# Kernel optimization log

Hardware: AMD Instinct MI355X
Metric: run time of the kernel (lower is better)

## Reference

```python
import jax, jax.numpy as jnp
import numpy as np

T, B, S, D = 512, 32, 512, 512
EPS = 1e-6  # LayerNorm eps


def _ln(x, g, b):
    m = jnp.mean(x, axis=-1, keepdims=True)
    v = jnp.mean((x - m) ** 2, axis=-1, keepdims=True)
    return g * (x - m) * jax.lax.rsqrt(v + EPS) + b


def setup_inputs() -> dict:
    key = jax.random.key(0)
    ks = jax.random.split(key, 10)
    sc = 1.0 / np.sqrt(D).astype(np.float32)
    return {
        "prev_layer": jax.random.normal(ks[0], (T, B, D), jnp.float32),
        "hidden": jax.random.normal(ks[1], (B, D), jnp.float32),
        "enc_output": jax.random.normal(ks[2], (B, S, D), jnp.float32),
        "memory_length": jax.random.randint(ks[3], (B,), 1, S + 1),
        # nn.Linear weights stored as [in, out] (transposed torch layout)
        "W_in": jax.random.normal(ks[4], (D, 3 * D), jnp.float32) * sc,
        "W_enc": jax.random.normal(ks[5], (D, D), jnp.float32) * sc,
        "W_attn_in": jax.random.normal(ks[6], (D, D), jnp.float32) * sc,
        "W_hidden": jax.random.normal(ks[7], (D, D), jnp.float32) * sc,
        "W_ctx": jax.random.normal(ks[8], (D, D), jnp.float32) * sc,
        # LayerNorm gains/biases (5 LNs)
        "g_pre": jnp.ones((3 * D,), jnp.float32), "b_pre": jnp.zeros((3 * D,), jnp.float32),
        "g_enc": jnp.ones((D,), jnp.float32), "b_enc": jnp.zeros((D,), jnp.float32),
        "g_attn": jnp.ones((D,), jnp.float32), "b_attn": jnp.zeros((D,), jnp.float32),
        "g_h": jnp.ones((D,), jnp.float32), "b_h": jnp.zeros((D,), jnp.float32),
        "g_c": jnp.ones((D,), jnp.float32), "b_c": jnp.zeros((D,), jnp.float32),
    }


def reference(prev_layer, hidden, enc_output, W_in, W_enc, W_attn_in, W_hidden,
              W_ctx, g_pre, b_pre, g_enc, b_enc, g_attn, b_attn, g_h, b_h,
              g_c, b_c, memory_length):
    d = prev_layer.shape[-1]
    sqrt_d = jnp.sqrt(jnp.asarray(d, prev_layer.dtype))
    # dropout is identity in eval mode
    preact = _ln(prev_layer @ W_in, g_pre, b_pre)          # [T,B,3D]
    pctx = _ln(enc_output @ W_enc, g_enc, b_enc)           # [B,S,D]
    z, h_gate, pl_t = jnp.split(preact, 3, axis=-1)
    z = jax.nn.sigmoid(z)
    h_gate = jax.nn.sigmoid(h_gate)

    # SRU-style linear recurrence: s_t = (1-z_t)*s_{t-1} + z_t*pl_t
    def step(h, zp):
        z_t, p_t = zp
        s = (1.0 - z_t) * h + z_t * p_t
        return s, s

    hidden_last, ss = jax.lax.scan(step, hidden, (z, pl_t))  # ss: [T,B,D]

    attn_in = _ln(ss @ W_attn_in, g_attn, b_attn)            # [T,B,D]
    align = jnp.einsum('tbd,bsd->bts', attn_in, pctx)        # [B,T,S]
    mask = jnp.arange(pctx.shape[1])[None, :] < memory_length[:, None]  # [B,S]
    align = jnp.where(mask[:, None, :], align, -jnp.inf)
    av = jax.nn.softmax(align / sqrt_d, axis=-1)             # [B,T,S]
    c = jnp.einsum('bts,bsd->tbd', av, pctx)                 # [T,B,D]
    attn_out = c / sqrt_d

    trans = _ln(ss @ W_hidden, g_h, b_h) + _ln(attn_out @ W_ctx, g_c, b_c)
    out = jnp.tanh(trans)
    out = (1.0 - h_gate) * out + h_gate * prev_layer         # [T,B,D]
    p_attn = jnp.transpose(av, (1, 0, 2))                    # [T,B,S]
    return out, hidden_last, p_attn
```

## Files before the change

### kernel.cpp

```cpp
#include <hip/hip_runtime.h>
#include <hip/hip_bf16.h>
#include <cmath>

#define T_ 512
#define B_ 32
#define S_ 512
#define D_ 512
#define D3_ 1536
#define NCH 16
#define CT (T_ / NCH)
static constexpr float LN_EPS = 1e-6f;
static constexpr float RSQRT_D = 0.044194173824159216f;

typedef __attribute__((ext_vector_type(8))) __bf16 bf16x8;
typedef __attribute__((ext_vector_type(4))) float f32x4;

struct __align__(8) bfx4 { __hip_bfloat16 x, y, z, w; };

__device__ __forceinline__ void g2l16(const void* g, void* l) {
    __builtin_amdgcn_global_load_lds(
        (const __attribute__((address_space(1))) unsigned int*)g,
        (__attribute__((address_space(3))) unsigned int*)l, 16, 0, 0);
}

__device__ __forceinline__ float xr_sum16(float v) {
    v += __shfl_xor(v, 1); v += __shfl_xor(v, 2);
    v += __shfl_xor(v, 4); v += __shfl_xor(v, 8); return v;
}
__device__ __forceinline__ float xr_max16(float v) {
    v = fmaxf(v, __shfl_xor(v, 1)); v = fmaxf(v, __shfl_xor(v, 2));
    v = fmaxf(v, __shfl_xor(v, 4)); v = fmaxf(v, __shfl_xor(v, 8)); return v;
}

__device__ __forceinline__ float sigmoidf_(float x) {
    return 1.f / (1.f + __expf(-x));
}
__device__ __forceinline__ float sigmoid_fast(float x) {
    return __fdividef(1.f, 1.f + __expf(-x));
}
__device__ __forceinline__ float tanh_fast(float x) {
    return 1.f - __fdividef(2.f, __expf(2.f * x) + 1.f);
}
__device__ __forceinline__ float bfu(unsigned short u) {
    unsigned int v = ((unsigned int)u) << 16;
    return __uint_as_float(v);
}

__global__ __launch_bounds__(256) void gemm_pre(
    const __hip_bfloat16* __restrict__ A,
    const __hip_bfloat16* __restrict__ Bw,
    __hip_bfloat16* __restrict__ preb,
    float2* __restrict__ part)
{
    __shared__ char smem[32768];

    const int lin = blockIdx.y * 12 + blockIdx.x;
    const int swz = (lin & 7) * 192 + (lin >> 3);
    const int bx = swz % 12, by = swz / 12;
    const int m0 = by * 128, n0 = bx * 128;
    const int tid = threadIdx.x, lane = tid & 63, w = tid >> 6;
    const int wm = (w >> 1) * 64, wn = (w & 1) * 64;
    const int srow = lane >> 2, skB = (lane & 3) * 16;
    const int q = lane >> 4, c = lane & 15;

    f32x4 acc[4][4];
#pragma unroll
    for (int i = 0; i < 4; i++)
#pragma unroll
        for (int j = 0; j < 4; j++) acc[i][j] = (f32x4)(0.0f);

    const char* ga0 = (const char*)(A + (long)(m0 + w * 16 + srow) * 512) + skB;
    const char* ga1 = (const char*)(A + (long)(m0 + (w + 4) * 16 + srow) * 512) + skB;
    const char* gb0 = (const char*)(Bw + (long)(n0 + w * 16 + srow) * 512) + skB;
    const char* gb1 = (const char*)(Bw + (long)(n0 + (w + 4) * 16 + srow) * 512) + skB;
    char* la0 = smem + w * 1024 + lane * 16;
    char* la1 = smem + (w + 4) * 1024 + lane * 16;
    char* lb0 = smem + 8192 + w * 1024 + lane * 16;
    char* lb1 = smem + 8192 + (w + 4) * 1024 + lane * 16;
    const char* Ar = smem + (wm + c) * 64 + q * 16;
    const char* Br = smem + 8192 + (wn + c) * 64 + q * 16;

    g2l16(ga0, la0);
    g2l16(ga1, la1);
    g2l16(gb0, lb0);
    g2l16(gb1, lb1);
    __syncthreads();

#pragma unroll
    for (int kk = 0; kk < 16; kk++) {
        const int cb = (kk & 1) << 14;
        const int nb = cb ^ 16384;
        if (kk < 15) {
            const long kb = (long)(kk + 1) * 64;
            g2l16(ga0 + kb, la0 + nb);
            g2l16(ga1 + kb, la1 + nb);
            g2l16(gb0 + kb, lb0 + nb);
            g2l16(gb1 + kb, lb1 + nb);
        }
        bf16x8 af[4], bfr[4];
#pragma unroll
        for (int i = 0; i < 4; i++) {
            af[i] = *(const bf16x8*)(Ar + cb + i * 1024);
            bfr[i] = *(const bf16x8*)(Br + cb + i * 1024);
        }
#pragma unroll
        for (int i = 0; i < 4; i++)
#pragma unroll
            for (int j = 0; j < 4; j++)
                acc[i][j] = __builtin_amdgcn_mfma_f32_16x16x32_bf16(
                    af[i], bfr[j], acc[i][j], 0, 0, 0);
        __syncthreads();
    }

    float2* sred = (float2*)smem;
#pragma unroll
    for (int i = 0; i < 4; i++)
#pragma unroll
        for (int r = 0; r < 4; r++) {
            float s = 0.f, qq = 0.f;
#pragma unroll
            for (int j = 0; j < 4; j++) {
                float v = acc[i][j][r]; s += v; qq += v * v;
            }
            s = xr_sum16(s); qq = xr_sum16(qq);
            if (c == 0) sred[(wm + i * 16 + q * 4 + r) * 2 + (w & 1)] =
                make_float2(s, qq);
        }
    __syncthreads();
    if ((w & 1) == 0 && c == 0) {
#pragma unroll
        for (int i = 0; i < 4; i++)
#pragma unroll
            for (int r = 0; r < 4; r++) {
                int row = wm + i * 16 + q * 4 + r;
                float2 a = sred[row * 2], b2 = sred[row * 2 + 1];
                part[(long)bx * 16384 + m0 + row] =
                    make_float2(a.x + b2.x, a.y + b2.y);
            }
    }
    __syncthreads();

    for (int p = 0; p < 2; p++) {
        if ((w >> 1) == p) {
#pragma unroll
            for (int i = 0; i < 4; i++)
#pragma unroll
                for (int j = 0; j < 4; j++)
#pragma unroll
                    for (int r = 0; r < 4; r++) {
                        int row = i * 16 + q * 4 + r;
                        int col = wn + j * 16 + c;
                        ((__hip_bfloat16*)smem)[row * 128 + col] =
                            __float2bfloat16(acc[i][j][r]);
                    }
        }
        __syncthreads();
#pragma unroll
        for (int rnd = 0; rnd < 4; rnd++) {
            int row = rnd * 16 + (tid >> 4);
            int ch = tid & 15;
            uint4 v = *(const uint4*)(smem + row * 256 + ch * 16);
            long grow = m0 + p * 64 + row;
            *(uint4*)((char*)preb + grow * 3072 + (long)n0 * 2 + ch * 16) = v;
        }
        __syncthreads();
    }
}

#define RC_BUF 34816
__device__ __forceinline__ void rows_core32(
    const __hip_bfloat16* A, long lda,
    const __hip_bfloat16* B, long ldb,
    char* smem, f32x4 (&acc)[2][8])
{
    const int tid = threadIdx.x, lane = tid & 63, w = tid >> 6;
#pragma unroll
    for (int m = 0; m < 2; m++)
#pragma unroll
        for (int j = 0; j < 8; j++) acc[m][j] = (f32x4)(0.0f);

    const char* ga = (const char*)(A + (long)(w * 16 + (lane >> 2)) * lda) + (lane & 3) * 16;
    char* la = smem + w * 1024 + lane * 16;
    const char* gb = (const char*)(B + (long)(w * 128 + (lane >> 2)) * ldb) + (lane & 3) * 16;
    char* lb = smem + 2048 + w * 8192 + lane * 16;
    const long ldbB16 = (long)ldb * 32;
    const char* Ar = smem + (lane & 15) * 64 + (lane >> 4) * 16;
    const char* Br = smem + 2048 + (w * 128 + (lane & 15)) * 64 + (lane >> 4) * 16;

    if (w < 2) g2l16(ga, la);
#pragma unroll
    for (int s = 0; s < 8; s++) g2l16(gb + s * ldbB16, lb + s * 1024);
    __syncthreads();

#pragma unroll
    for (int kk = 0; kk < 16; kk++) {
        const int cb = (kk & 1) * RC_BUF;
        const int nb = ((kk & 1) ^ 1) * RC_BUF;
        if (kk < 15) {
            const long kb = (long)(kk + 1) * 64;
            if (w < 2) g2l16(ga + kb, la + nb);
#pragma unroll
            for (int s = 0; s < 8; s++)
                g2l16(gb + kb + s * ldbB16, lb + nb + s * 1024);
        }
        bf16x8 af[2], bfr[8];
#pragma unroll
        for (int m = 0; m < 2; m++) af[m] = *(const bf16x8*)(Ar + cb + m * 1024);
#pragma unroll
        for (int j = 0; j < 8; j++) bfr[j] = *(const bf16x8*)(Br + cb + j * 1024);
#pragma unroll
        for (int m = 0; m < 2; m++)
#pragma unroll
            for (int j = 0; j < 8; j++)
                acc[m][j] = __builtin_amdgcn_mfma_f32_16x16x32_bf16(
                    af[m], bfr[j], acc[m][j], 0, 0, 0);
        __syncthreads();
    }
}

__global__ __launch_bounds__(256, 2) void gemm_ln(
    const __hip_bfloat16* __restrict__ A, long lda,
    const __hip_bfloat16* __restrict__ W,
    const float* __restrict__ g, const float* __restrict__ bb,
    __hip_bfloat16* __restrict__ out)
{
    __shared__ char smem[69632];
    const long m0 = (long)blockIdx.y * 32;
    f32x4 acc[2][8];
    rows_core32(A + m0 * lda, lda, W, 512, smem, acc);

    const int tid = threadIdx.x, lane = tid & 63, w = tid >> 6;
    const int q = lane >> 4, c = lane & 15;
    float2* sred = (float2*)smem;
#pragma unroll
    for (int m = 0; m < 2; m++)
#pragma unroll
        for (int r = 0; r < 4; r++) {
            float s = 0.f, qq = 0.f;
#pragma unroll
            for (int j = 0; j < 8; j++) {
                float v = acc[m][j][r]; s += v; qq += v * v;
            }
            s = xr_sum16(s); qq = xr_sum16(qq);
            if (c == 0) sred[(m * 16 + q * 4 + r) * 4 + w] = make_float2(s, qq);
        }
    __syncthreads();
    float mean[2][4], rstd[2][4];
#pragma unroll
    for (int m = 0; m < 2; m++)
#pragma unroll
        for (int r = 0; r < 4; r++) {
            int row = m * 16 + q * 4 + r;
            float s = 0.f, qq = 0.f;
#pragma unroll
            for (int ww = 0; ww < 4; ww++) {
                float2 t = sred[row * 4 + ww]; s += t.x; qq += t.y;
            }
            float mn = s * (1.f / 512);
            mean[m][r] = mn;
            rstd[m][r] = rsqrtf(qq * (1.f / 512) - mn * mn + LN_EPS);
        }
    __syncthreads();
#pragma unroll
    for (int m = 0; m < 2; m++)
#pragma unroll
        for (int j = 0; j < 8; j++) {
            int col = w * 128 + j * 16 + c;
            float gv = g[col], bv = bb[col];
#pragma unroll
            for (int r = 0; r < 4; r++) {
                int row = m * 16 + q * 4 + r;
                float v = (acc[m][j][r] - mean[m][r]) * rstd[m][r] * gv + bv;
                ((__hip_bfloat16*)smem)[row * 512 + col] = __float2bfloat16(v);
            }
        }
    __syncthreads();
#pragma unroll
    for (int rnd = 0; rnd < 8; rnd++) {
        int row = rnd * 4 + w;
        uint4 v = *(const uint4*)(smem + row * 1024 + lane * 16);
        *(uint4*)((char*)out + (m0 + row) * 1024 + lane * 16) = v;
    }
}

__global__ __launch_bounds__(256, 2) void gemm_attn(
    const __hip_bfloat16* __restrict__ attninb,
    const __hip_bfloat16* __restrict__ pctxb,
    const int* __restrict__ mlen,
    float* __restrict__ pattn, __hip_bfloat16* __restrict__ pattnb)
{
    __shared__ char smem[69632];
    const int b = blockIdx.z;
    const long t0 = (long)blockIdx.y * 32;
    f32x4 acc[2][8];
    rows_core32(attninb + (long)b * 512 + t0 * 16384, 16384,
                pctxb + (long)b * 262144, 512, smem, acc);

    const int tid = threadIdx.x, lane = tid & 63, w = tid >> 6;
    const int q = lane >> 4, c = lane & 15;
    const int len = mlen[b];
    float* sred = (float*)smem;

#pragma unroll
    for (int m = 0; m < 2; m++)
#pragma unroll
        for (int r = 0; r < 4; r++) {
            float mx = -INFINITY;
#pragma unroll
            for (int j = 0; j < 8; j++) {
                int col = w * 128 + j * 16 + c;
                float v = acc[m][j][r] * RSQRT_D;
                acc[m][j][r] = v;
                if (col < len) mx = fmaxf(mx, v);
            }
            mx = xr_max16(mx);
            if (c == 0) sred[(m * 16 + q * 4 + r) * 4 + w] = mx;
        }
    __syncthreads();
    float rmax[2][4];
#pragma unroll
    for (int m = 0; m < 2; m++)
#pragma unroll
        for (int r = 0; r < 4; r++) {
            int row = m * 16 + q * 4 + r;
            rmax[m][r] = fmaxf(fmaxf(sred[row * 4], sred[row * 4 + 1]),
                               fmaxf(sred[row * 4 + 2], sred[row * 4 + 3]));
        }
    __syncthreads();
#pragma unroll
    for (int m = 0; m < 2; m++)
#pragma unroll
        for (int r = 0; r < 4; r++) {
            float s = 0.f;
#pragma unroll
            for (int j = 0; j < 8; j++) {
                int col = w * 128 + j * 16 + c;
                float e = (col < len) ? __expf(acc[m][j][r] - rmax[m][r]) : 0.f;
                acc[m][j][r] = e; s += e;
            }
            s = xr_sum16(s);
            if (c == 0) sred[(m * 16 + q * 4 + r) * 4 + w] = s;
        }
    __syncthreads();
    float rinv[2][4];
#pragma unroll
    for (int m = 0; m < 2; m++)
#pragma unroll
        for (int r = 0; r < 4; r++) {
            int row = m * 16 + q * 4 + r;
            rinv[m][r] = 1.f / (sred[row * 4] + sred[row * 4 + 1] +
                                sred[row * 4 + 2] + sred[row * 4 + 3]);
        }
    __syncthreads();

#pragma unroll
    for (int m = 0; m < 2; m++)
#pragma unroll
        for (int j = 0; j < 8; j++)
#pragma unroll
            for (int r = 0; r < 4; r++) {
                int row = m * 16 + q * 4 + r;
                int col = w * 128 + j * 16 + c;
                float p = acc[m][j][r] * rinv[m][r];
                acc[m][j][r] = p;
                pattn[((t0 + row) * 32 + b) * 512 + col] = p;
                ((__hip_bfloat16*)smem)[row * 512 + col] = __float2bfloat16(p);
            }
    __syncthreads();
#pragma unroll
    for (int rnd = 0; rnd < 8; rnd++) {
        int row = rnd * 4 + w;
        uint4 v = *(const uint4*)(smem + row * 1024 + lane * 16);
        *(uint4*)((char*)pattnb + ((t0 + row) * 32 + b) * 1024 + lane * 16) = v;
    }
}

__global__ __launch_bounds__(256, 2) void gemm_av(
    const __hip_bfloat16* __restrict__ pattnb,
    const __hip_bfloat16* __restrict__ pctxT,
    __hip_bfloat16* __restrict__ attnoutb)
{
    __shared__ char smem[69632];
    const int b = blockIdx.z;
    const long t0 = (long)blockIdx.y * 32;
    f32x4 acc[2][8];
    rows_core32(pattnb + (long)b * 512 + t0 * 16384, 16384,
                pctxT + (long)b * 262144, 512, smem, acc);

    const int tid = threadIdx.x, lane = tid & 63, w = tid >> 6;
    const int q = lane >> 4, c = lane & 15;
#pragma unroll
    for (int m = 0; m < 2; m++)
#pragma unroll
        for (int j = 0; j < 8; j++)
#pragma unroll
            for (int r = 0; r < 4; r++) {
                int row = m * 16 + q * 4 + r;
                int col = w * 128 + j * 16 + c;
                ((__hip_bfloat16*)smem)[row * 512 + col] =
                    __float2bfloat16(acc[m][j][r] * RSQRT_D);
            }
    __syncthreads();
#pragma unroll
    for (int rnd = 0; rnd < 8; rnd++) {
        int row = rnd * 4 + w;
        uint4 v = *(const uint4*)(smem + row * 1024 + lane * 16);
        *(uint4*)((char*)attnoutb + ((t0 + row) * 32 + b) * 1024 + lane * 16) = v;
    }
}

__global__ __launch_bounds__(256, 2) void gemm_fin(
    const __hip_bfloat16* __restrict__ attnoutb,
    const __hip_bfloat16* __restrict__ Wc,
    const __hip_bfloat16* __restrict__ h1n,
    const __hip_bfloat16* __restrict__ preb,
    const float2* __restrict__ stats,
    const float* __restrict__ g_c, const float* __restrict__ b_c,
    const float* __restrict__ g_pre, const float* __restrict__ b_pre,
    const float* __restrict__ prev, float* __restrict__ out)
{
    __shared__ char smem[69632];
    const long m0 = (long)blockIdx.y * 32;
    f32x4 acc[2][8];
    rows_core32(attnoutb + m0 * 512, 512, Wc, 512, smem, acc);

    const int tid = threadIdx.x, lane = tid & 63, w = tid >> 6;
    const int q = lane >> 4, c = lane & 15;
    float2* sred = (float2*)smem;
#pragma unroll
    for (int m = 0; m < 2; m++)
#pragma unroll
        for (int r = 0; r < 4; r++) {
            float s = 0.f, qq = 0.f;
#pragma unroll
            for (int j = 0; j < 8; j++) {
                float v = acc[m][j][r]; s += v; qq += v * v;
            }
            s = xr_sum16(s); qq = xr_sum16(qq);
            if (c == 0) sred[(m * 16 + q * 4 + r) * 4 + w] = make_float2(s, qq);
        }
    __syncthreads();
    float mean[2][4], rstd[2][4];
#pragma unroll
    for (int m = 0; m < 2; m++)
#pragma unroll
        for (int r = 0; r < 4; r++) {
            int row = m * 16 + q * 4 + r;
            float s = 0.f, qq = 0.f;
#pragma unroll
            for (int ww = 0; ww < 4; ww++) {
                float2 t = sred[row * 4 + ww]; s += t.x; qq += t.y;
            }
            float mn = s * (1.f / 512);
            mean[m][r] = mn;
            rstd[m][r] = rsqrtf(qq * (1.f / 512) - mn * mn + LN_EPS);
        }
    __syncthreads();

    float* t2s = (float*)smem;
#pragma unroll
    for (int m = 0; m < 2; m++)
#pragma unroll
        for (int j = 0; j < 8; j++) {
            int col = w * 128 + j * 16 + c;
            float gv = g_c[col], bv = b_c[col];
#pragma unroll
            for (int r = 0; r < 4; r++) {
                int row = m * 16 + q * 4 + r;
                t2s[row * 512 + col] =
                    (acc[m][j][r] - mean[m][r]) * rstd[m][r] * gv + bv;
            }
        }
    __syncthreads();

#pragma unroll
    for (int ch = 0; ch < 16; ch++) {
        int f4 = ch * 256 + tid;
        int row = f4 >> 7;
        long rowg = m0 + row;
        int col = (f4 & 127) * 4;
        float4 t2 = ((const float4*)t2s)[f4];
        ushort4 h1 = *(const ushort4*)((const char*)h1n + rowg * 1024 + col * 2);
        ushort4 hr = *(const ushort4*)((const char*)preb + rowg * 3072 + 1024 + col * 2);
        float4 pv = *(const float4*)(prev + rowg * 512 + col);
        float4 gp = *(const float4*)(g_pre + 512 + col);
        float4 bp = *(const float4*)(b_pre + 512 + col);
        float2 sh = stats[rowg];
        auto fuse = [&](unsigned short h1u, unsigned short hru, float t2v,
                        float pvv, float gpv, float bpv) -> float {
            float hg = sigmoid_fast((bfu(hru) - sh.x) * sh.y * gpv + bpv);
            float th = tanh_fast(bfu(h1u) + t2v);
            return (1.f - hg) * th + hg * pvv;
        };
        float4 o;
        o.x = fuse(h1.x, hr.x, t2.x, pv.x, gp.x, bp.x);
        o.y = fuse(h1.y, hr.y, t2.y, pv.y, gp.y, bp.y);
        o.z = fuse(h1.z, hr.z, t2.z, pv.z, gp.z, bp.z);
        o.w = fuse(h1.w, hr.w, t2.w, pv.w, gp.w, bp.w);
        *(float4*)(out + rowg * 512 + col) = o;
    }
}

__global__ __launch_bounds__(256) void cvt4(
    const float* __restrict__ x, __hip_bfloat16* __restrict__ y, int n4)
{
    int i = blockIdx.x * 256 + threadIdx.x;
    if (i >= n4) return;
    float4 v = ((const float4*)x)[i];
    bfx4 o;
    o.x = __float2bfloat16(v.x); o.y = __float2bfloat16(v.y);
    o.z = __float2bfloat16(v.z); o.w = __float2bfloat16(v.w);
    ((bfx4*)y)[i] = o;
}

__global__ __launch_bounds__(256) void wtrans(
    const float* __restrict__ w0, const float* __restrict__ w1,
    const float* __restrict__ w2, const float* __restrict__ w3,
    const float* __restrict__ w4, __hip_bfloat16* __restrict__ WT)
{
    int z = blockIdx.z;
    const float* W; long off; int N;
    if (z == 0)      { W = w0; off = 0;                N = 1536; }
    else if (z == 1) { W = w1; off = 786432;           N = 512; }
    else if (z == 2) { W = w2; off = 786432 + 262144;  N = 512; }
    else if (z == 3) { W = w3; off = 786432 + 524288;  N = 512; }
    else             { W = w4; off = 786432 + 786432;  N = 512; }
    int n0 = blockIdx.x * 32, k0 = blockIdx.y * 32;
    if (n0 >= N) return;
    __shared__ float t[32][33];
    int tx = threadIdx.x & 31, ty = threadIdx.x >> 5;
#pragma unroll
    for (int i = 0; i < 4; i++)
        t[ty + i * 8][tx] = W[(long)(k0 + ty + i * 8) * N + n0 + tx];
    __syncthreads();
    __hip_bfloat16* O = WT + off;
#pragma unroll
    for (int i = 0; i < 4; i++)
        O[(long)(n0 + ty + i * 8) * 512 + k0 + tx] =
            __float2bfloat16(t[tx][ty + i * 8]);
}

__global__ __launch_bounds__(256) void ptrans(
    const __hip_bfloat16* __restrict__ src, __hip_bfloat16* __restrict__ dst)
{
    long boff = (long)blockIdx.z * (S_ * D_);
    int d0 = blockIdx.x * 32, s0 = blockIdx.y * 32;
    __shared__ __hip_bfloat16 t[32][34];
    int tx = threadIdx.x & 31, ty = threadIdx.x >> 5;
#pragma unroll
    for (int i = 0; i < 4; i++)
        t[ty + i * 8][tx] = src[boff + (long)(s0 + ty + i * 8) * D_ + d0 + tx];
    __syncthreads();
#pragma unroll
    for (int i = 0; i < 4; i++)
        dst[boff + (long)(d0 + ty + i * 8) * S_ + s0 + tx] = t[tx][ty + i * 8];
}

__global__ __launch_bounds__(256) void stats_fin(
    const float2* __restrict__ part, float2* __restrict__ stats)
{
    int r = blockIdx.x * 256 + threadIdx.x;
    float s = 0.f, qq = 0.f;
#pragma unroll
    for (int cb = 0; cb < 12; cb++) {
        float2 v = part[(long)cb * 16384 + r]; s += v.x; qq += v.y;
    }
    float m = s * (1.f / 1536);
    float rs = rsqrtf(qq * (1.f / 1536) - m * m + LN_EPS);
    stats[r] = make_float2(m, rs);
}

__global__ __launch_bounds__(256) void scan_part1(
    const __hip_bfloat16* __restrict__ preb, const float2* __restrict__ stats,
    const float* __restrict__ gpre, const float* __restrict__ bpre,
    float* __restrict__ Ap, float* __restrict__ Bp)
{
    int idx = blockIdx.x * 256 + threadIdx.x;
    int b = idx >> 9, d = idx & 511;
    int ch = blockIdx.y;
    float gz = gpre[d], bz = bpre[d];
    float gp = gpre[1024 + d], bpv = bpre[1024 + d];
    float A = 1.f, s = 0.f;
    for (int t = ch * CT; t < (ch + 1) * CT; t++) {
        long row = (long)t * 32 + b;
        float2 st = stats[row];
        float zr = __bfloat162float(preb[row * 1536 + d]);
        float pr = __bfloat162float(preb[row * 1536 + 1024 + d]);
        float z = sigmoidf_((zr - st.x) * st.y * gz + bz);
        float pl = (pr - st.x) * st.y * gp + bpv;
        float a = 1.f - z;
        A *= a;
        s = a * s + z * pl;
    }
    Ap[ch * 16384 + idx] = A;
    Bp[ch * 16384 + idx] = s;
}

__global__ __launch_bounds__(256) void scan_part2(
    const float* __restrict__ Ap, const float* __restrict__ Bp,
    const float* __restrict__ h0, float* __restrict__ sin_,
    float* __restrict__ hlast)
{
    int idx = blockIdx.x * 256 + threadIdx.x;
    float s = h0[idx];
    for (int ch = 0; ch < NCH; ch++) {
        sin_[ch * 16384 + idx] = s;
        s = Ap[ch * 16384 + idx] * s + Bp[ch * 16384 + idx];
    }
    hlast[idx] = s;
}

__global__ __launch_bounds__(256) void scan_part3(
    const __hip_bfloat16* __restrict__ preb, const float2* __restrict__ stats,
    const float* __restrict__ gpre, const float* __restrict__ bpre,
    const float* __restrict__ sin_, __hip_bfloat16* __restrict__ ssb)
{
    int idx = blockIdx.x * 256 + threadIdx.x;
    int b = idx >> 9, d = idx & 511;
    int ch = blockIdx.y;
    float gz = gpre[d], bz = bpre[d];
    float gp = gpre[1024 + d], bpv = bpre[1024 + d];
    float s = sin_[ch * 16384 + idx];
    for (int t = ch * CT; t < (ch + 1) * CT; t++) {
        long row = (long)t * 32 + b;
        float2 st = stats[row];
        float zr = __bfloat162float(preb[row * 1536 + d]);
        float pr = __bfloat162float(preb[row * 1536 + 1024 + d]);
        float z = sigmoidf_((zr - st.x) * st.y * gz + bz);
        float pl = (pr - st.x) * st.y * gp + bpv;
        s += z * (pl - s);
        ssb[(long)t * 16384 + idx] = __float2bfloat16(s);
    }
}

extern "C" void kernel_launch(void* const* d_in, const int* in_sizes, int n_in,
                              void* d_out, int out_size, void* d_ws, size_t ws_size,
                              hipStream_t stream) {
    const float* prev  = (const float*)d_in[0];
    const float* hid0  = (const float*)d_in[1];
    const float* enc   = (const float*)d_in[2];
    const int*   mlen  = (const int*)  d_in[3];
    const float* W_in  = (const float*)d_in[4];
    const float* W_enc = (const float*)d_in[5];
    const float* W_att = (const float*)d_in[6];
    const float* W_hid = (const float*)d_in[7];
    const float* W_ctx = (const float*)d_in[8];
    const float* g_pre = (const float*)d_in[9];
    const float* b_pre = (const float*)d_in[10];
    const float* g_enc = (const float*)d_in[11];
    const float* b_enc = (const float*)d_in[12];
    const float* g_att = (const float*)d_in[13];
    const float* b_att = (const float*)d_in[14];
    const float* g_h   = (const float*)d_in[15];
    const float* b_h   = (const float*)d_in[16];
    const float* g_c   = (const float*)d_in[17];
    const float* b_c   = (const float*)d_in[18];

    float* out   = (float*)d_out;
    float* hlast = out + (long)T_ * B_ * D_;
    float* pattn = hlast + (long)B_ * D_;

    char* ws = (char*)d_ws;
    __hip_bfloat16* preb    = (__hip_bfloat16*)(ws);
    __hip_bfloat16* WT      = (__hip_bfloat16*)(ws + 50331648);
    __hip_bfloat16* prevb   = (__hip_bfloat16*)(ws + 54525952);
    __hip_bfloat16* encb    = (__hip_bfloat16*)(ws + 71303168);
    __hip_bfloat16* pctxb   = (__hip_bfloat16*)(ws + 88080384);
    __hip_bfloat16* pctxT   = (__hip_bfloat16*)(ws + 104857600);
    __hip_bfloat16* ssb     = (__hip_bfloat16*)(ws + 121634816);
    __hip_bfloat16* attninb = (__hip_bfloat16*)(ws + 138412032);
    __hip_bfloat16* pattnb  = (__hip_bfloat16*)(ws + 155189248);
    __hip_bfloat16* attnoutb= (__hip_bfloat16*)(ws + 171966464);
    __hip_bfloat16* h1n     = (__hip_bfloat16*)(ws + 188743680);
    float2* part            = (float2*)(ws + 205520896);
    float2* stats           = (float2*)(ws + 207093760);
    float* scanA            = (float*)(ws + 207224832);
    float* scanB            = (float*)(ws + 208273408);
    float* sinb             = (float*)(ws + 209321984);

    const __hip_bfloat16* W_encT = WT + 786432;
    const __hip_bfloat16* W_attT = WT + 786432 + 262144;
    const __hip_bfloat16* W_hidT = WT + 786432 + 524288;
    const __hip_bfloat16* W_ctxT = WT + 786432 + 786432;

    dim3 blk(256);

    cvt4<<<8192, blk, 0, stream>>>(prev, prevb, 2097152);
    cvt4<<<8192, blk, 0, stream>>>(enc, encb, 2097152);
    wtrans<<<dim3(48, 16, 5), blk, 0, stream>>>(W_in, W_enc, W_att, W_hid,
                                                W_ctx, WT);

    gemm_pre<<<dim3(12, 128), blk, 0, stream>>>(prevb, WT, preb, part);
    stats_fin<<<64, blk, 0, stream>>>(part, stats);

    scan_part1<<<dim3(64, NCH), blk, 0, stream>>>(preb, stats, g_pre, b_pre,
                                                  scanA, scanB);
    scan_part2<<<64, blk, 0, stream>>>(scanA, scanB, hid0, sinb, hlast);
    scan_part3<<<dim3(64, NCH), blk, 0, stream>>>(preb, stats, g_pre, b_pre,
                                                  sinb, ssb);

    gemm_ln<<<dim3(1, 512), blk, 0, stream>>>(encb, 512, W_encT, g_enc, b_enc,
                                              pctxb);
    ptrans<<<dim3(16, 16, 32), blk, 0, stream>>>(pctxb, pctxT);

    gemm_ln<<<dim3(1, 512), blk, 0, stream>>>(ssb, 512, W_attT, g_att, b_att,
                                              attninb);

    gemm_attn<<<dim3(1, 16, 32), blk, 0, stream>>>(attninb, pctxb, mlen,
                                                   pattn, pattnb);

    gemm_av<<<dim3(1, 16, 32), blk, 0, stream>>>(pattnb, pctxT, attnoutb);

    gemm_ln<<<dim3(1, 512), blk, 0, stream>>>(ssb, 512, W_hidT, g_h, b_h, h1n);

    gemm_fin<<<dim3(1, 512), blk, 0, stream>>>(attnoutb, W_ctxT, h1n, preb,
                                               stats, g_c, b_c, g_pre, b_pre,
                                               prev, out);
}
```

Baseline: 436.4 us.

## Load MFMA operands directly from global memory instead of staging through LDS

The shared 32-row GEMM core used to stage A and B tiles into double-buffered LDS with global_load_lds and synchronise every k-step. It now reads bf16x8 fragments straight from global memory into registers and drops all barriers, and the kernels' LDS allocations shrink to what the epilogues need. The aim is to remove barrier and LDS traffic overhead and raise occupancy. The cost is no explicit prefetch or reuse across waves: every wave loads the shared A rows itself, and the global reads are strided per lane, so the loop relies on cache hits and latency hiding.

```diff
diff --git a/kernel.cpp b/kernel.cpp
--- a/kernel.cpp
+++ b/kernel.cpp
@@ -167,54 +167,39 @@
     }
 }
 
-#define RC_BUF 34816
 __device__ __forceinline__ void rows_core32(
-    const __hip_bfloat16* A, long lda,
-    const __hip_bfloat16* B, long ldb,
-    char* smem, f32x4 (&acc)[2][8])
-{
-    const int tid = threadIdx.x, lane = tid & 63, w = tid >> 6;
+    const __hip_bfloat16* __restrict__ A, long lda,
+    const __hip_bfloat16* __restrict__ B, long ldb,
+    f32x4 (&acc)[2][8])
+{
+    const int lane = threadIdx.x & 63, w = threadIdx.x >> 6;
+    const int fr = lane & 15;
+    const int kq = lane >> 4;
 #pragma unroll
     for (int m = 0; m < 2; m++)
 #pragma unroll
         for (int j = 0; j < 8; j++) acc[m][j] = (f32x4)(0.0f);
 
-    const char* ga = (const char*)(A + (long)(w * 16 + (lane >> 2)) * lda) + (lane & 3) * 16;
-    char* la = smem + w * 1024 + lane * 16;
-    const char* gb = (const char*)(B + (long)(w * 128 + (lane >> 2)) * ldb) + (lane & 3) * 16;
-    char* lb = smem + 2048 + w * 8192 + lane * 16;
+    const char* a0 = (const char*)(A + (long)fr * lda) + kq * 16;
+    const char* a1 = (const char*)(A + (long)(16 + fr) * lda) + kq * 16;
+    const char* b0 = (const char*)(B + (long)(w * 128 + fr) * ldb) + kq * 16;
     const long ldbB16 = (long)ldb * 32;
-    const char* Ar = smem + (lane & 15) * 64 + (lane >> 4) * 16;
-    const char* Br = smem + 2048 + (w * 128 + (lane & 15)) * 64 + (lane >> 4) * 16;
-
-    if (w < 2) g2l16(ga, la);
-#pragma unroll
-    for (int s = 0; s < 8; s++) g2l16(gb + s * ldbB16, lb + s * 1024);
-    __syncthreads();
 
 #pragma unroll
     for (int kk = 0; kk < 16; kk++) {
-        const int cb = (kk & 1) * RC_BUF;
-        const int nb = ((kk & 1) ^ 1) * RC_BUF;
-        if (kk < 15) {
-            const long kb = (long)(kk + 1) * 64;
-            if (w < 2) g2l16(ga + kb, la + nb);
-#pragma unroll
-            for (int s = 0; s < 8; s++)
-                g2l16(gb + kb + s * ldbB16, lb + nb + s * 1024);
-        }
+        const long kb = (long)kk * 64;
         bf16x8 af[2], bfr[8];
-#pragma unroll
-        for (int m = 0; m < 2; m++) af[m] = *(const bf16x8*)(Ar + cb + m * 1024);
-#pragma unroll
-        for (int j = 0; j < 8; j++) bfr[j] = *(const bf16x8*)(Br + cb + j * 1024);
+        af[0] = *(const bf16x8*)(a0 + kb);
+        af[1] = *(const bf16x8*)(a1 + kb);
+#pragma unroll
+        for (int j = 0; j < 8; j++)
+            bfr[j] = *(const bf16x8*)(b0 + kb + j * ldbB16);
 #pragma unroll
         for (int m = 0; m < 2; m++)
 #pragma unroll
             for (int j = 0; j < 8; j++)
                 acc[m][j] = __builtin_amdgcn_mfma_f32_16x16x32_bf16(
                     af[m], bfr[j], acc[m][j], 0, 0, 0);
-        __syncthreads();
     }
 }
 
@@ -224,10 +209,10 @@
     const float* __restrict__ g, const float* __restrict__ bb,
     __hip_bfloat16* __restrict__ out)
 {
-    __shared__ char smem[69632];
+    __shared__ char smem[32768];
     const long m0 = (long)blockIdx.y * 32;
     f32x4 acc[2][8];
-    rows_core32(A + m0 * lda, lda, W, 512, smem, acc);
+    rows_core32(A + m0 * lda, lda, W, 512, acc);
 
     const int tid = threadIdx.x, lane = tid & 63, w = tid >> 6;
     const int q = lane >> 4, c = lane & 15;
@@ -289,12 +274,12 @@
     const int* __restrict__ mlen,
     float* __restrict__ pattn, __hip_bfloat16* __restrict__ pattnb)
 {
-    __shared__ char smem[69632];
+    __shared__ char smem[32768];
     const int b = blockIdx.z;
     const long t0 = (long)blockIdx.y * 32;
     f32x4 acc[2][8];
     rows_core32(attninb + (long)b * 512 + t0 * 16384, 16384,
-                pctxb + (long)b * 262144, 512, smem, acc);
+                pctxb + (long)b * 262144, 512, acc);
 
     const int tid = threadIdx.x, lane = tid & 63, w = tid >> 6;
     const int q = lane >> 4, c = lane & 15;
@@ -380,12 +365,12 @@
     const __hip_bfloat16* __restrict__ pctxT,
     __hip_bfloat16* __restrict__ attnoutb)
 {
-    __shared__ char smem[69632];
+    __shared__ char smem[32768];
     const int b = blockIdx.z;
     const long t0 = (long)blockIdx.y * 32;
     f32x4 acc[2][8];
     rows_core32(pattnb + (long)b * 512 + t0 * 16384, 16384,
-                pctxT + (long)b * 262144, 512, smem, acc);
+                pctxT + (long)b * 262144, 512, acc);
 
     const int tid = threadIdx.x, lane = tid & 63, w = tid >> 6;
     const int q = lane >> 4, c = lane & 15;
@@ -419,10 +404,10 @@
     const float* __restrict__ g_pre, const float* __restrict__ b_pre,
     const float* __restrict__ prev, float* __restrict__ out)
 {
-    __shared__ char smem[69632];
+    __shared__ char smem[65536];
     const long m0 = (long)blockIdx.y * 32;
     f32x4 acc[2][8];
-    rows_core32(attnoutb + m0 * 512, 512, Wc, 512, smem, acc);
+    rows_core32(attnoutb + m0 * 512, 512, Wc, 512, acc);
 
     const int tid = threadIdx.x, lane = tid & 63, w = tid >> 6;
     const int q = lane >> 4, c = lane & 15;
```

New measurement: 523.5 us. 20.0% more time.

## Replace 32-row full-width GEMM+LN kernels with 128x128 tiled GEMM plus split LN

Applied to the files above, without the earlier changes.

The row-complete GEMM+LayerNorm kernels, which computed 32x512 tiles, are replaced by a generic 128x128 tile GEMM. It emits per-row partial sums, followed by a stats reduction kernel and a separate LN-apply pass. The attention-value GEMM and the final context GEMM use the same tile kernel, and the final LN/tanh/gate fusion moves into an elementwise epilogue kernel. This is meant to improve operand reuse and MFMA efficiency per block, at the cost of extra launches and additional read/write passes over the bf16 outputs.

```diff
diff --git a/kernel.cpp b/kernel.cpp
--- a/kernel.cpp
+++ b/kernel.cpp
@@ -16,6 +16,7 @@
 typedef __attribute__((ext_vector_type(4))) float f32x4;
 
 struct __align__(8) bfx4 { __hip_bfloat16 x, y, z, w; };
+struct __align__(16) u16x8 { unsigned short h[8]; };
 
 __device__ __forceinline__ void g2l16(const void* g, void* l) {
     __builtin_amdgcn_global_load_lds(
@@ -167,8 +168,141 @@
     }
 }
 
+__global__ __launch_bounds__(256) void g128(
+    const __hip_bfloat16* __restrict__ A, long ldaE,
+    const __hip_bfloat16* __restrict__ Bw, long bStrideZ,
+    __hip_bfloat16* __restrict__ out, long outStrideB,
+    float2* __restrict__ part, float scale, int swizzle)
+{
+    __shared__ char smem[32768];
+    int bx, by;
+    if (gridDim.z > 1) {
+        bx = blockIdx.x; by = blockIdx.y;
+        A += (long)blockIdx.z * 512;
+        Bw += (long)blockIdx.z * bStrideZ;
+        out += (long)blockIdx.z * 512;
+    } else if (swizzle) {
+        const int nwg = gridDim.x * gridDim.y;
+        const int lin = blockIdx.y * gridDim.x + blockIdx.x;
+        const int cpx = nwg >> 3;
+        const int swz = (lin & 7) * cpx + (lin >> 3);
+        bx = swz % gridDim.x; by = swz / gridDim.x;
+    } else { bx = blockIdx.x; by = blockIdx.y; }
+
+    const int m0 = by * 128, n0 = bx * 128;
+    const int tid = threadIdx.x, lane = tid & 63, w = tid >> 6;
+    const int wm = (w >> 1) * 64, wn = (w & 1) * 64;
+    const int srow = lane >> 2, skB = (lane & 3) * 16;
+    const int q = lane >> 4, c = lane & 15;
+
+    f32x4 acc[4][4];
+#pragma unroll
+    for (int i = 0; i < 4; i++)
+#pragma unroll
+        for (int j = 0; j < 4; j++) acc[i][j] = (f32x4)(0.0f);
+
+    const char* ga0 = (const char*)(A + (long)(m0 + w * 16 + srow) * ldaE) + skB;
+    const char* ga1 = (const char*)(A + (long)(m0 + (w + 4) * 16 + srow) * ldaE) + skB;
+    const char* gb0 = (const char*)(Bw + (long)(n0 + w * 16 + srow) * 512) + skB;
+    const char* gb1 = (const char*)(Bw + (long)(n0 + (w + 4) * 16 + srow) * 512) + skB;
+    char* la0 = smem + w * 1024 + lane * 16;
+    char* la1 = smem + (w + 4) * 1024 + lane * 16;
+    char* lb0 = smem + 8192 + w * 1024 + lane * 16;
+    char* lb1 = smem + 8192 + (w + 4) * 1024 + lane * 16;
+    const char* Ar = smem + (wm + c) * 64 + q * 16;
+    const char* Br = smem + 8192 + (wn + c) * 64 + q * 16;
+
+    g2l16(ga0, la0);
+    g2l16(ga1, la1);
+    g2l16(gb0, lb0);
+    g2l16(gb1, lb1);
+    __syncthreads();
+
+#pragma unroll
+    for (int kk = 0; kk < 16; kk++) {
+        const int cb = (kk & 1) << 14;
+        const int nb = cb ^ 16384;
+        if (kk < 15) {
+            const long kb = (long)(kk + 1) * 64;
+            g2l16(ga0 + kb, la0 + nb);
+            g2l16(ga1 + kb, la1 + nb);
+            g2l16(gb0 + kb, lb0 + nb);
+            g2l16(gb1 + kb, lb1 + nb);
+        }
+        bf16x8 af[4], bfr[4];
+#pragma unroll
+        for (int i = 0; i < 4; i++) {
+            af[i] = *(const bf16x8*)(Ar + cb + i * 1024);
+            bfr[i] = *(const bf16x8*)(Br + cb + i * 1024);
+        }
+#pragma unroll
+        for (int i = 0; i < 4; i++)
+#pragma unroll
+            for (int j = 0; j < 4; j++)
+                acc[i][j] = __builtin_amdgcn_mfma_f32_16x16x32_bf16(
+                    af[i], bfr[j], acc[i][j], 0, 0, 0);
+        __syncthreads();
+    }
+
+    if (part) {
+        float2* sred = (float2*)smem;
+#pragma unroll
+        for (int i = 0; i < 4; i++)
+#pragma unroll
+            for (int r = 0; r < 4; r++) {
+                float s = 0.f, qq = 0.f;
+#pragma unroll
+                for (int j = 0; j < 4; j++) {
+                    float v = acc[i][j][r]; s += v; qq += v * v;
+                }
+                s = xr_sum16(s); qq = xr_sum16(qq);
+                if (c == 0) sred[(wm + i * 16 + q * 4 + r) * 2 + (w & 1)] =
+                    make_float2(s, qq);
+            }
+        __syncthreads();
+        if ((w & 1) == 0 && c == 0) {
+#pragma unroll
+            for (int i = 0; i < 4; i++)
+#pragma unroll
+                for (int r = 0; r < 4; r++) {
+                    int row = wm + i * 16 + q * 4 + r;
+                    float2 a = sred[row * 2], b2 = sred[row * 2 + 1];
+                    part[(long)bx * 16384 + m0 + row] =
+                        make_float2(a.x + b2.x, a.y + b2.y);
+                }
+        }
+        __syncthreads();
+    }
+
+    for (int p = 0; p < 2; p++) {
+        if ((w >> 1) == p) {
+#pragma unroll
+            for (int i = 0; i < 4; i++)
+#pragma unroll
+                for (int j = 0; j < 4; j++)
+#pragma unroll
+                    for (int r = 0; r < 4; r++) {
+                        int row = i * 16 + q * 4 + r;
+                        int col = wn + j * 16 + c;
+                        ((__hip_bfloat16*)smem)[row * 128 + col] =
+                            __float2bfloat16(acc[i][j][r] * scale);
+                    }
+        }
+        __syncthreads();
+#pragma unroll
+        for (int rnd = 0; rnd < 4; rnd++) {
+            int row = rnd * 16 + (tid >> 4);
+            int ch = tid & 15;
+            uint4 v = *(const uint4*)(smem + row * 256 + ch * 16);
+            long grow = m0 + p * 64 + row;
+            *(uint4*)((char*)out + grow * outStrideB + (long)n0 * 2 + ch * 16) = v;
+        }
+        __syncthreads();
+    }
+}
+
 #define RC_BUF 34816
-__device__ __forceinline__ void rows_core32(
+__device__ __forceinline__ void rows_core32_lds(
     const __hip_bfloat16* A, long lda,
     const __hip_bfloat16* B, long ldb,
     char* smem, f32x4 (&acc)[2][8])
@@ -218,71 +352,6 @@
     }
 }
 
-__global__ __launch_bounds__(256, 2) void gemm_ln(
-    const __hip_bfloat16* __restrict__ A, long lda,
-    const __hip_bfloat16* __restrict__ W,
-    const float* __restrict__ g, const float* __restrict__ bb,
-    __hip_bfloat16* __restrict__ out)
-{
-    __shared__ char smem[69632];
-    const long m0 = (long)blockIdx.y * 32;
-    f32x4 acc[2][8];
-    rows_core32(A + m0 * lda, lda, W, 512, smem, acc);
-
-    const int tid = threadIdx.x, lane = tid & 63, w = tid >> 6;
-    const int q = lane >> 4, c = lane & 15;
-    float2* sred = (float2*)smem;
-#pragma unroll
-    for (int m = 0; m < 2; m++)
-#pragma unroll
-        for (int r = 0; r < 4; r++) {
-            float s = 0.f, qq = 0.f;
-#pragma unroll
-            for (int j = 0; j < 8; j++) {
-                float v = acc[m][j][r]; s += v; qq += v * v;
-            }
-            s = xr_sum16(s); qq = xr_sum16(qq);
-            if (c == 0) sred[(m * 16 + q * 4 + r) * 4 + w] = make_float2(s, qq);
-        }
-    __syncthreads();
-    float mean[2][4], rstd[2][4];
-#pragma unroll
-    for (int m = 0; m < 2; m++)
-#pragma unroll
-        for (int r = 0; r < 4; r++) {
-            int row = m * 16 + q * 4 + r;
-            float s = 0.f, qq = 0.f;
-#pragma unroll
-            for (int ww = 0; ww < 4; ww++) {
-                float2 t = sred[row * 4 + ww]; s += t.x; qq += t.y;
-            }
-            float mn = s * (1.f / 512);
-            mean[m][r] = mn;
-            rstd[m][r] = rsqrtf(qq * (1.f / 512) - mn * mn + LN_EPS);
-        }
-    __syncthreads();
-#pragma unroll
-    for (int m = 0; m < 2; m++)
-#pragma unroll
-        for (int j = 0; j < 8; j++) {
-            int col = w * 128 + j * 16 + c;
-            float gv = g[col], bv = bb[col];
-#pragma unroll
-            for (int r = 0; r < 4; r++) {
-                int row = m * 16 + q * 4 + r;
-                float v = (acc[m][j][r] - mean[m][r]) * rstd[m][r] * gv + bv;
-                ((__hip_bfloat16*)smem)[row * 512 + col] = __float2bfloat16(v);
-            }
-        }
-    __syncthreads();
-#pragma unroll
-    for (int rnd = 0; rnd < 8; rnd++) {
-        int row = rnd * 4 + w;
-        uint4 v = *(const uint4*)(smem + row * 1024 + lane * 16);
-        *(uint4*)((char*)out + (m0 + row) * 1024 + lane * 16) = v;
-    }
-}
-
 __global__ __launch_bounds__(256, 2) void gemm_attn(
     const __hip_bfloat16* __restrict__ attninb,
     const __hip_bfloat16* __restrict__ pctxb,
@@ -293,8 +362,8 @@
     const int b = blockIdx.z;
     const long t0 = (long)blockIdx.y * 32;
     f32x4 acc[2][8];
-    rows_core32(attninb + (long)b * 512 + t0 * 16384, 16384,
-                pctxb + (long)b * 262144, 512, smem, acc);
+    rows_core32_lds(attninb + (long)b * 512 + t0 * 16384, 16384,
+                    pctxb + (long)b * 262144, 512, smem, acc);
 
     const int tid = threadIdx.x, lane = tid & 63, w = tid >> 6;
     const int q = lane >> 4, c = lane & 15;
@@ -375,128 +444,81 @@
     }
 }
 
-__global__ __launch_bounds__(256, 2) void gemm_av(
-    const __hip_bfloat16* __restrict__ pattnb,
-    const __hip_bfloat16* __restrict__ pctxT,
-    __hip_bfloat16* __restrict__ attnoutb)
-{
-    __shared__ char smem[69632];
-    const int b = blockIdx.z;
-    const long t0 = (long)blockIdx.y * 32;
-    f32x4 acc[2][8];
-    rows_core32(pattnb + (long)b * 512 + t0 * 16384, 16384,
-                pctxT + (long)b * 262144, 512, smem, acc);
-
-    const int tid = threadIdx.x, lane = tid & 63, w = tid >> 6;
-    const int q = lane >> 4, c = lane & 15;
-#pragma unroll
-    for (int m = 0; m < 2; m++)
-#pragma unroll
-        for (int j = 0; j < 8; j++)
-#pragma unroll
-            for (int r = 0; r < 4; r++) {
-                int row = m * 16 + q * 4 + r;
-                int col = w * 128 + j * 16 + c;
-                ((__hip_bfloat16*)smem)[row * 512 + col] =
-                    __float2bfloat16(acc[m][j][r] * RSQRT_D);
-            }
-    __syncthreads();
-#pragma unroll
-    for (int rnd = 0; rnd < 8; rnd++) {
-        int row = rnd * 4 + w;
-        uint4 v = *(const uint4*)(smem + row * 1024 + lane * 16);
-        *(uint4*)((char*)attnoutb + ((t0 + row) * 32 + b) * 1024 + lane * 16) = v;
-    }
-}
-
-__global__ __launch_bounds__(256, 2) void gemm_fin(
-    const __hip_bfloat16* __restrict__ attnoutb,
-    const __hip_bfloat16* __restrict__ Wc,
-    const __hip_bfloat16* __restrict__ h1n,
+__global__ __launch_bounds__(256) void stats4(
+    const float2* __restrict__ part, float2* __restrict__ st)
+{
+    int r = blockIdx.x * 256 + threadIdx.x;
+    float s = 0.f, qq = 0.f;
+#pragma unroll
+    for (int cb = 0; cb < 4; cb++) {
+        float2 v = part[(long)cb * 16384 + r]; s += v.x; qq += v.y;
+    }
+    float m = s * (1.f / 512);
+    float rs = rsqrtf(qq * (1.f / 512) - m * m + LN_EPS);
+    st[r] = make_float2(m, rs);
+}
+
+__global__ __launch_bounds__(256) void ln_apply(
+    __hip_bfloat16* __restrict__ x, const float2* __restrict__ st,
+    const float* __restrict__ g, const float* __restrict__ bb)
+{
+    int i = blockIdx.x * 256 + threadIdx.x;
+    int row = i >> 6;
+    int c0 = (i & 63) * 8;
+    float2 s = st[row];
+    u16x8 v = *(const u16x8*)((const char*)x + (long)i * 16);
+    float4 g0 = *(const float4*)(g + c0), g1 = *(const float4*)(g + c0 + 4);
+    float4 b0 = *(const float4*)(bb + c0), b1 = *(const float4*)(bb + c0 + 4);
+    float gv[8] = {g0.x, g0.y, g0.z, g0.w, g1.x, g1.y, g1.z, g1.w};
+    float bv[8] = {b0.x, b0.y, b0.z, b0.w, b1.x, b1.y, b1.z, b1.w};
+#pragma unroll
+    for (int k = 0; k < 8; k++) {
+        float f = (bfu(v.h[k]) - s.x) * s.y * gv[k] + bv[k];
+        v.h[k] = __hip_bfloat16_raw(__float2bfloat16(f)).x;
+    }
+    *(u16x8*)((char*)x + (long)i * 16) = v;
+}
+
+__global__ __launch_bounds__(256) void fin_ep(
+    const __hip_bfloat16* __restrict__ h2r, const __hip_bfloat16* __restrict__ h1r,
     const __hip_bfloat16* __restrict__ preb,
-    const float2* __restrict__ stats,
+    const float2* __restrict__ st_c, const float2* __restrict__ st_h,
+    const float2* __restrict__ st_p,
     const float* __restrict__ g_c, const float* __restrict__ b_c,
+    const float* __restrict__ g_h, const float* __restrict__ b_h,
     const float* __restrict__ g_pre, const float* __restrict__ b_pre,
     const float* __restrict__ prev, float* __restrict__ out)
 {
-    __shared__ char smem[69632];
-    const long m0 = (long)blockIdx.y * 32;
-    f32x4 acc[2][8];
-    rows_core32(attnoutb + m0 * 512, 512, Wc, 512, smem, acc);
-
-    const int tid = threadIdx.x, lane = tid & 63, w = tid >> 6;
-    const int q = lane >> 4, c = lane & 15;
-    float2* sred = (float2*)smem;
-#pragma unroll
-    for (int m = 0; m < 2; m++)
-#pragma unroll
-        for (int r = 0; r < 4; r++) {
-            float s = 0.f, qq = 0.f;
-#pragma unroll
-            for (int j = 0; j < 8; j++) {
-                float v = acc[m][j][r]; s += v; qq += v * v;
-            }
-            s = xr_sum16(s); qq = xr_sum16(qq);
-            if (c == 0) sred[(m * 16 + q * 4 + r) * 4 + w] = make_float2(s, qq);
-        }
-    __syncthreads();
-    float mean[2][4], rstd[2][4];
-#pragma unroll
-    for (int m = 0; m < 2; m++)
-#pragma unroll
-        for (int r = 0; r < 4; r++) {
-            int row = m * 16 + q * 4 + r;
-            float s = 0.f, qq = 0.f;
-#pragma unroll
-            for (int ww = 0; ww < 4; ww++) {
-                float2 t = sred[row * 4 + ww]; s += t.x; qq += t.y;
-            }
-            float mn = s * (1.f / 512);
-            mean[m][r] = mn;
-            rstd[m][r] = rsqrtf(qq * (1.f / 512) - mn * mn + LN_EPS);
-        }
-    __syncthreads();
-
-    float* t2s = (float*)smem;
-#pragma unroll
-    for (int m = 0; m < 2; m++)
-#pragma unroll
-        for (int j = 0; j < 8; j++) {
-            int col = w * 128 + j * 16 + c;
-            float gv = g_c[col], bv = b_c[col];
-#pragma unroll
-            for (int r = 0; r < 4; r++) {
-                int row = m * 16 + q * 4 + r;
-                t2s[row * 512 + col] =
-                    (acc[m][j][r] - mean[m][r]) * rstd[m][r] * gv + bv;
-            }
-        }
-    __syncthreads();
-
+    const long m0 = (long)blockIdx.x * 32;
+    const int tid = threadIdx.x;
 #pragma unroll
     for (int ch = 0; ch < 16; ch++) {
         int f4 = ch * 256 + tid;
         int row = f4 >> 7;
         long rowg = m0 + row;
         int col = (f4 & 127) * 4;
-        float4 t2 = ((const float4*)t2s)[f4];
-        ushort4 h1 = *(const ushort4*)((const char*)h1n + rowg * 1024 + col * 2);
+        ushort4 h2 = *(const ushort4*)((const char*)h2r + rowg * 1024 + col * 2);
+        ushort4 h1 = *(const ushort4*)((const char*)h1r + rowg * 1024 + col * 2);
         ushort4 hr = *(const ushort4*)((const char*)preb + rowg * 3072 + 1024 + col * 2);
         float4 pv = *(const float4*)(prev + rowg * 512 + col);
+        float4 gc = *(const float4*)(g_c + col), bc = *(const float4*)(b_c + col);
+        float4 gh = *(const float4*)(g_h + col), bh = *(const float4*)(b_h + col);
         float4 gp = *(const float4*)(g_pre + 512 + col);
         float4 bp = *(const float4*)(b_pre + 512 + col);
-        float2 sh = stats[rowg];
-        auto fuse = [&](unsigned short h1u, unsigned short hru, float t2v,
-                        float pvv, float gpv, float bpv) -> float {
-            float hg = sigmoid_fast((bfu(hru) - sh.x) * sh.y * gpv + bpv);
-            float th = tanh_fast(bfu(h1u) + t2v);
-            return (1.f - hg) * th + hg * pvv;
+        float2 sc = st_c[rowg], sh = st_h[rowg], sp = st_p[rowg];
+        auto fuse = [&](unsigned short h2u, unsigned short h1u, unsigned short hru,
+                        float pvv, float gcv, float bcv, float ghv, float bhv,
+                        float gpv, float bpv) -> float {
+            float t2 = (bfu(h2u) - sc.x) * sc.y * gcv + bcv;
+            float t1 = (bfu(h1u) - sh.x) * sh.y * ghv + bhv;
+            float hg = sigmoid_fast((bfu(hru) - sp.x) * sp.y * gpv + bpv);
+            return (1.f - hg) * tanh_fast(t1 + t2) + hg * pvv;
         };
         float4 o;
-        o.x = fuse(h1.x, hr.x, t2.x, pv.x, gp.x, bp.x);
-        o.y = fuse(h1.y, hr.y, t2.y, pv.y, gp.y, bp.y);
-        o.z = fuse(h1.z, hr.z, t2.z, pv.z, gp.z, bp.z);
-        o.w = fuse(h1.w, hr.w, t2.w, pv.w, gp.w, bp.w);
+        o.x = fuse(h2.x, h1.x, hr.x, pv.x, gc.x, bc.x, gh.x, bh.x, gp.x, bp.x);
+        o.y = fuse(h2.y, h1.y, hr.y, pv.y, gc.y, bc.y, gh.y, bh.y, gp.y, bp.y);
+        o.z = fuse(h2.z, h1.z, hr.z, pv.z, gc.z, bc.z, gh.z, bh.z, gp.z, bp.z);
+        o.w = fuse(h2.w, h1.w, hr.w, pv.w, gc.w, bc.w, gh.w, bh.w, gp.w, bp.w);
         *(float4*)(out + rowg * 512 + col) = o;
     }
 }
@@ -677,6 +699,12 @@
     float* scanA            = (float*)(ws + 207224832);
     float* scanB            = (float*)(ws + 208273408);
     float* sinb             = (float*)(ws + 209321984);
+    float2* stats_enc       = (float2*)(ws + 210370560);
+    float2* stats_att       = (float2*)(ws + 210501632);
+    float2* stats_h         = (float2*)(ws + 210632704);
+    float2* stats_c         = (float2*)(ws + 210763776);
+
+    __hip_bfloat16* h2raw = pattnb;
 
     const __hip_bfloat16* W_encT = WT + 786432;
     const __hip_bfloat16* W_attT = WT + 786432 + 262144;
@@ -699,21 +727,33 @@
     scan_part3<<<dim3(64, NCH), blk, 0, stream>>>(preb, stats, g_pre, b_pre,
                                                   sinb, ssb);
 
-    gemm_ln<<<dim3(1, 512), blk, 0, stream>>>(encb, 512, W_encT, g_enc, b_enc,
-                                              pctxb);
+    g128<<<dim3(4, 128), blk, 0, stream>>>(encb, 512, W_encT, 0, pctxb, 1024,
+                                           part, 1.f, 1);
+    stats4<<<64, blk, 0, stream>>>(part, stats_enc);
+    ln_apply<<<4096, blk, 0, stream>>>(pctxb, stats_enc, g_enc, b_enc);
     ptrans<<<dim3(16, 16, 32), blk, 0, stream>>>(pctxb, pctxT);
 
-    gemm_ln<<<dim3(1, 512), blk, 0, stream>>>(ssb, 512, W_attT, g_att, b_att,
-                                              attninb);
+    g128<<<dim3(4, 128), blk, 0, stream>>>(ssb, 512, W_attT, 0, attninb, 1024,
+                                           part, 1.f, 1);
+    stats4<<<64, blk, 0, stream>>>(part, stats_att);
+    ln_apply<<<4096, blk, 0, stream>>>(attninb, stats_att, g_att, b_att);
 
     gemm_attn<<<dim3(1, 16, 32), blk, 0, stream>>>(attninb, pctxb, mlen,
                                                    pattn, pattnb);
 
-    gemm_av<<<dim3(1, 16, 32), blk, 0, stream>>>(pattnb, pctxT, attnoutb);
-
-    gemm_ln<<<dim3(1, 512), blk, 0, stream>>>(ssb, 512, W_hidT, g_h, b_h, h1n);
-
-    gemm_fin<<<dim3(1, 512), blk, 0, stream>>>(attnoutb, W_ctxT, h1n, preb,
-                                               stats, g_c, b_c, g_pre, b_pre,
-                                               prev, out);
-}
+    g128<<<dim3(4, 4, 32), blk, 0, stream>>>(pattnb, 16384, pctxT, 262144,
+                                             attnoutb, 32768, nullptr,
+                                             RSQRT_D, 0);
+
+    g128<<<dim3(4, 128), blk, 0, stream>>>(ssb, 512, W_hidT, 0, h1n, 1024,
+                                           part, 1.f, 1);
+    stats4<<<64, blk, 0, stream>>>(part, stats_h);
+
+    g128<<<dim3(4, 128), blk, 0, stream>>>(attnoutb, 512, W_ctxT, 0, h2raw,
+                                           1024, part, 1.f, 1);
+    stats4<<<64, blk, 0, stream>>>(part, stats_c);
+
+    fin_ep<<<512, blk, 0, stream>>>(h2raw, h1n, preb, stats_c, stats_h, stats,
+                                    g_c, b_c, g_h, b_h, g_pre, b_pre, prev,
+                                    out);
+}
```

Measured after the change: 448.5 us. 1.03x slower.
